# Optimization experiments

Measured on AMD Instinct MI355X. Metric: run time of the kernel, lower is better.

## Reference

```python
import jax, jax.numpy as jnp
import numpy as np

EMBED_DIM = 256
NUM_HEADS = 8
NUM_QUERIES = 448
TEMPERATURE = 10000.0
SCALE = 100.0
EPS = 1e-5
B, N = 1, 512
NUM_CLASSES = 91


def box_rel_encoding(src_boxes, tgt_boxes, eps=EPS):
    # boxes: [B, N, 4] as (cx, cy, w, h)
    xy1, wh1 = src_boxes[..., :2], src_boxes[..., 2:]
    xy2, wh2 = tgt_boxes[..., :2], tgt_boxes[..., 2:]
    delta_xy = jnp.abs(xy1[..., :, None, :] - xy2[..., None, :, :])          # [B,N,N,2]
    delta_xy = jnp.log(delta_xy / (wh1[..., :, None, :] + eps) + 1.0)
    delta_wh = jnp.log((wh1[..., :, None, :] + eps) / (wh2[..., None, :, :] + eps))
    return jnp.concatenate([delta_xy, delta_wh], axis=-1)                    # [B,N,N,4]


def get_sine_pos_embed(pos, num_pos_feats, temperature=TEMPERATURE, scale=SCALE):
    # pos: [..., C]; returns [..., C * num_pos_feats]; exchange_xy=False
    dim_t = jnp.arange(num_pos_feats, dtype=pos.dtype)
    dim_t = temperature ** (2.0 * jnp.floor(dim_t / 2.0) / num_pos_feats)
    x = pos[..., None] * scale / dim_t                                        # [...,C,F]
    emb = jnp.stack([jnp.sin(x[..., 0::2]), jnp.cos(x[..., 1::2])], axis=-1)  # [...,C,F/2,2]
    emb = emb.reshape(x.shape)                                                # [...,C,F]
    return emb.reshape(pos.shape[:-1] + (pos.shape[-1] * num_pos_feats,))


def setup_inputs() -> dict:
    key = jax.random.key(0)
    ks = jax.random.split(key, 9)
    s = 0.02
    return {
        "src_boxes": jax.random.uniform(ks[0], (B, N, 4), jnp.float32, 0.05, 0.95),
        "pred_logits": jax.random.normal(ks[1], (B, N, NUM_CLASSES), jnp.float32),
        "rank_emb": jax.random.normal(ks[2], (NUM_QUERIES, EMBED_DIM), jnp.float32) * s,
        "pre_W": jax.random.normal(ks[3], (EMBED_DIM, EMBED_DIM), jnp.float32) * s,
        "pre_b": jax.random.normal(ks[4], (EMBED_DIM,), jnp.float32) * s,
        "post_W": jax.random.normal(ks[5], (EMBED_DIM, 2 * EMBED_DIM), jnp.float32) * s,
        "post_b": jax.random.normal(ks[6], (EMBED_DIM,), jnp.float32) * s,
        "attn_W": jax.random.normal(ks[7], (NUM_HEADS, EMBED_DIM), jnp.float32) * s,
        "attn_b": jax.random.normal(ks[8], (NUM_HEADS,), jnp.float32) * s,
        "layer_idx": 2,
    }


def reference(src_boxes, pred_logits, rank_emb, pre_W, pre_b, post_W, post_b, attn_W, attn_b, layer_idx):
    num_denoising = N - NUM_QUERIES
    # --- no-grad block: pairwise box relation + rank-ordered gather reorder ---
    base = box_rel_encoding(src_boxes, src_boxes)                            # [B,N,N,4]
    scores = jnp.max(jax.nn.sigmoid(pred_logits[:, num_denoising:]), axis=-1)  # [B,Q]
    order = jnp.argsort(-scores, axis=1)                                      # descending  [B,Q]
    rank_indices = jnp.broadcast_to(jnp.arange(N, dtype=order.dtype), (B, N))
    rank_indices = rank_indices.at[:, num_denoising:].set(order + num_denoising)
    nr = base[:, num_denoising:, num_denoising:]                              # [B,Q,Q,4]
    nr = jnp.take_along_axis(nr, order[:, :, None, None], axis=1)
    nr = jnp.take_along_axis(nr, order[:, None, :, None], axis=2)
    base = base.at[:, num_denoising:, num_denoising:].set(nr)
    base = jax.lax.stop_gradient(base)
    # --- sine positional embedding of relation: [B,N,N,EMBED_DIM] ---
    pos = get_sine_pos_embed(base, EMBED_DIM // 4)
    # --- rank-aware relation: embedding -> pre linear -> pairwise sum ---
    normal_rank = rank_emb @ pre_W.T + pre_b                                  # [Q,E]
    rank_rel = jnp.zeros((B, N, EMBED_DIM), src_boxes.dtype)
    rank_rel = rank_rel.at[:, num_denoising:].set(normal_rank[None])
    rank_rel = rank_rel[:, :, None, :] + rank_rel[:, None, :, :]              # [B,N,N,E]
    relation = jnp.concatenate([pos, rank_rel], axis=-1)                      # [B,N,N,2E]
    relation = relation @ post_W.T + post_b                                   # [B,N,N,E]
    attn = jax.nn.relu(relation @ attn_W.T + attn_b)                          # [B,N,N,H]
    attn = jnp.transpose(attn, (0, 3, 1, 2))                                  # [B,H,N,N]
    return attn, rank_indices
```

## Files before the change

### kernel.cpp

```cpp
#include <hip/hip_runtime.h>
#include <hip/hip_bf16.h>
#include <math.h>

#define NN 512
#define NQ 448
#define ND 64
#define NC 91
#define ED 256
#define NH 8

typedef __attribute__((ext_vector_type(8))) short bf16x8;
typedef __attribute__((ext_vector_type(4))) float f32x4;

struct FreqArg { float fr[32]; };

__device__ int   g_perm[NN];
__device__ float g_c0[NH];
__device__ float g_afull[NN * NH];
__device__ __align__(16) unsigned short g_WB[8 * 64 * 8];

__device__ inline unsigned short f2bfbits(float x) {
    __hip_bfloat16 h = __float2bfloat16(x);
    union { __hip_bfloat16 b; unsigned short u; } cv; cv.b = h; return cv.u;
}

__global__ __launch_bounds__(512) void precomp(const float* __restrict__ logits,
                                               const float* __restrict__ attn_W,
                                               const float* __restrict__ attn_b,
                                               const float* __restrict__ post_W,
                                               const float* __restrict__ post_b,
                                               const float* __restrict__ pre_W,
                                               const float* __restrict__ pre_b,
                                               const float* __restrict__ rank_emb,
                                               float* __restrict__ out2) {
    __shared__ float sAW[ED];
    __shared__ float sFold[512];
    __shared__ float sU2[512];
    __shared__ float sU[ED];
    __shared__ float sc[NQ];
    __shared__ float sB2a;
    int bid = blockIdx.x, t = threadIdx.x;

    if (bid < NH) {
        int h = bid;
        if (t < ED) sAW[t] = attn_W[h * ED + t];
        __syncthreads();

        float m = 0.f;
        const float* pw = post_W + t;
#pragma unroll 16
        for (int c = 0; c < ED; ++c) m = fmaf(sAW[c], pw[(size_t)c * 512], m);
        sFold[t] = m;
        __syncthreads();

        {
            int e = t & 255, half = t >> 8;
            float acc = 0.f;
            const float* pwc = pre_W + (size_t)(half * 128) * ED + e;
#pragma unroll 16
            for (int dl = 0; dl < 128; ++dl)
                acc = fmaf(sFold[256 + half * 128 + dl], pwc[(size_t)dl * ED], acc);
            sU2[half * 256 + e] = acc;
        }
        if (t < 64) {
            float v = 0.f;
#pragma unroll
            for (int k = 0; k < 4; ++k) v = fmaf(sAW[t + 64 * k], post_b[t + 64 * k], v);
            for (int off = 32; off > 0; off >>= 1) v += __shfl_down(v, off, 64);
            if (t == 0) g_c0[h] = attn_b[h] + v;
        } else if (t < 128) {
            int l = t - 64;
            float v = 0.f;
#pragma unroll
            for (int k = 0; k < 4; ++k) v = fmaf(sFold[256 + l + 64 * k], pre_b[l + 64 * k], v);
            for (int off = 32; off > 0; off >>= 1) v += __shfl_down(v, off, 64);
            if (l == 0) sB2a = v;
        }
        if (t < 256) {
            int s = t >> 5, g = (t >> 3) & 3, ii = t & 7;
            int d = g * 64 + ((s * 4 + (ii >> 1)) << 1) + (ii & 1);
            g_WB[s * 512 + (g * 16 + h) * 8 + ii] = f2bfbits(sFold[d]);
        }
        if (t < ND) g_afull[t * NH + h] = 0.f;
        __syncthreads();
        if (t < ED) sU[t] = sU2[t] + sU2[256 + t];
        __syncthreads();

        float b2a = sB2a;
        for (int pass = 0; pass < 14; ++pass) {
            int q = pass * 32 + (t >> 4);
            int sub = t & 15;
            const float* re = rank_emb + (size_t)q * ED;
            float a = 0.f;
#pragma unroll
            for (int kk = 0; kk < 16; ++kk) a = fmaf(re[sub + 16 * kk], sU[sub + 16 * kk], a);
            a += __shfl_xor(a, 1, 64);
            a += __shfl_xor(a, 2, 64);
            a += __shfl_xor(a, 4, 64);
            a += __shfl_xor(a, 8, 64);
            if (sub == 0) g_afull[(size_t)(ND + q) * NH + h] = b2a + a;
        }
    } else {
        for (int v = t; v < 4096; v += 512) {
            int lane = (v >> 3) & 63;
            if ((lane & 15) >= NH) g_WB[v] = 0;
        }
        int W = t >> 6, lane = t & 63;
        for (int qi = 0; qi < 56; ++qi) {
            int q = W * 56 + qi;
            const float* row = logits + (size_t)(ND + q) * NC;
            float m = (lane < NC) ? row[lane] : -INFINITY;
            int c2 = lane + 64;
            if (c2 < NC) m = fmaxf(m, row[c2]);
            for (int off = 32; off > 0; off >>= 1) m = fmaxf(m, __shfl_down(m, off, 64));
            if (lane == 0) sc[q] = m;
        }
        __syncthreads();
        if (t < NQ) {
            float s1 = sc[t];
            int r1 = 0;
            for (int j = 0; j < NQ; ++j) {
                float sj = sc[j];
                r1 += ((sj > s1) || (sj == s1 && j < t)) ? 1 : 0;
            }
            g_perm[ND + r1] = ND + t;
            out2[ND + r1] = (float)(ND + t);
        }
        if (t < ND) {
            g_perm[t] = t;
            out2[t] = (float)t;
        }
    }
}

__global__ __launch_bounds__(256) void relation_main(const float* __restrict__ boxes,
                                                     FreqArg fa,
                                                     float* __restrict__ out) {
    __shared__ bf16x8 sWB[8][64];
    int t = threadIdx.x;
    ((uint4*)sWB)[t]       = ((const uint4*)g_WB)[t];
    ((uint4*)sWB)[t + 256] = ((const uint4*)g_WB)[t + 256];
    __syncthreads();

    int wave = t >> 6, lane = t & 63;
    int g = lane >> 4, r = lane & 15;
    int i = blockIdx.x >> 3;
    int j = ((blockIdx.x & 7) << 6) + (wave << 4) + r;

    int pi = i, pj = j;
    if (i >= ND && j >= ND) { pi = g_perm[i]; pj = g_perm[j]; }
    float4 b1 = ((const float4*)boxes)[pi];
    float4 b2 = ((const float4*)boxes)[pj];
    const float eps = 1e-5f;
    float ft;
    if (g == 0)      ft = logf(fabsf(b1.x - b2.x) / (b1.z + eps) + 1.0f);
    else if (g == 1) ft = logf(fabsf(b1.y - b2.y) / (b1.w + eps) + 1.0f);
    else if (g == 2) ft = logf((b1.z + eps) / (b2.z + eps));
    else             ft = logf((b1.w + eps) / (b2.w + eps));

    f32x4 acc = {0.f, 0.f, 0.f, 0.f};
#pragma unroll
    for (int s = 0; s < 8; ++s) {
        bf16x8 bfrag;
#pragma unroll
        for (int a = 0; a < 4; ++a) {
            float rev = ft * fa.fr[s * 4 + a];
            rev -= floorf(rev);
            float sv = __builtin_amdgcn_sinf(rev);
            float cv = __builtin_amdgcn_cosf(rev);
            bfrag[2 * a]     = (short)f2bfbits(sv);
            bfrag[2 * a + 1] = (short)f2bfbits(cv);
        }
        acc = __builtin_amdgcn_mfma_f32_16x16x32_bf16(sWB[s][lane], bfrag, acc, 0, 0, 0);
    }

    if (g < 2) {
        float4 cb = *(const float4*)(g_c0 + g * 4);
        float4 ai = *(const float4*)(g_afull + i * NH + g * 4);
        float4 aj = *(const float4*)(g_afull + j * NH + g * 4);
        const float* cbp = (const float*)&cb;
        const float* aip = (const float*)&ai;
        const float* ajp = (const float*)&aj;
#pragma unroll
        for (int q = 0; q < 4; ++q) {
            int h = g * 4 + q;
            float v = acc[q] + cbp[q] + aip[q] + ajp[q];
            v = v > 0.f ? v : 0.f;
            out[(size_t)h * (NN * NN) + i * NN + j] = v;
        }
    }
}

extern "C" void kernel_launch(void* const* d_in, const int* in_sizes, int n_in,
                              void* d_out, int out_size, void* d_ws, size_t ws_size,
                              hipStream_t stream) {
    const float* boxes    = (const float*)d_in[0];
    const float* logits   = (const float*)d_in[1];
    const float* rank_emb = (const float*)d_in[2];
    const float* pre_W    = (const float*)d_in[3];
    const float* pre_b    = (const float*)d_in[4];
    const float* post_W   = (const float*)d_in[5];
    const float* post_b   = (const float*)d_in[6];
    const float* attn_W   = (const float*)d_in[7];
    const float* attn_b   = (const float*)d_in[8];
    float* out = (float*)d_out;

    precomp<<<NH + 1, 512, 0, stream>>>(logits, attn_W, attn_b, post_W, post_b,
                                        pre_W, pre_b, rank_emb,
                                        out + (size_t)NH * NN * NN);

    FreqArg fa;
    for (int k = 0; k < 32; ++k)
        fa.fr[k] = (float)(100.0 / (2.0 * M_PI) / pow(10000.0, (double)k / 32.0));

    relation_main<<<4096, 256, 0, stream>>>(boxes, fa, out);
}
```

Baseline: 51.03 us.

## Split precompute across more blocks and move rank projection into tiled main kernel

Measured after the change: 59.90 us. +17.4%, slower.

```diff
diff --git a/kernel.cpp b/kernel.cpp
--- a/kernel.cpp
+++ b/kernel.cpp
@@ -16,7 +16,8 @@
 
 __device__ int   g_perm[NN];
 __device__ float g_c0[NH];
-__device__ float g_afull[NN * NH];
+__device__ float g_u[NH * ED];
+__device__ float g_b2a[NH];
 __device__ __align__(16) unsigned short g_WB[8 * 64 * 8];
 
 __device__ inline unsigned short f2bfbits(float x) {
@@ -24,87 +25,65 @@
     union { __hip_bfloat16 b; unsigned short u; } cv; cv.b = h; return cv.u;
 }
 
-__global__ __launch_bounds__(512) void precomp(const float* __restrict__ logits,
-                                               const float* __restrict__ attn_W,
-                                               const float* __restrict__ attn_b,
-                                               const float* __restrict__ post_W,
-                                               const float* __restrict__ post_b,
-                                               const float* __restrict__ pre_W,
-                                               const float* __restrict__ pre_b,
-                                               const float* __restrict__ rank_emb,
-                                               float* __restrict__ out2) {
+__global__ __launch_bounds__(512) void k1(const float* __restrict__ logits,
+                                          const float* __restrict__ attn_W,
+                                          const float* __restrict__ attn_b,
+                                          const float* __restrict__ post_W,
+                                          const float* __restrict__ post_b,
+                                          const float* __restrict__ pre_W,
+                                          const float* __restrict__ pre_b,
+                                          float* __restrict__ out2) {
     __shared__ float sAW[ED];
-    __shared__ float sFold[512];
-    __shared__ float sU2[512];
-    __shared__ float sU[ED];
+    __shared__ float sHalf[2][ED];
+    __shared__ float sW[ED];
+    __shared__ float sU2[2 * ED];
     __shared__ float sc[NQ];
-    __shared__ float sB2a;
     int bid = blockIdx.x, t = threadIdx.x;
 
-    if (bid < NH) {
-        int h = bid;
+    if (bid < 16) {
+        int h = bid >> 1, part = bid & 1;
         if (t < ED) sAW[t] = attn_W[h * ED + t];
         __syncthreads();
-
+        int dl = t & 255, cp = t >> 8;
         float m = 0.f;
-        const float* pw = post_W + t;
+        const float* pw = post_W + (size_t)(cp * 128) * 512 + part * 256 + dl;
 #pragma unroll 16
-        for (int c = 0; c < ED; ++c) m = fmaf(sAW[c], pw[(size_t)c * 512], m);
-        sFold[t] = m;
+        for (int ci = 0; ci < 128; ++ci) m = fmaf(sAW[cp * 128 + ci], pw[(size_t)ci * 512], m);
+        sHalf[cp][dl] = m;
         __syncthreads();
 
-        {
+        if (part == 0) {
+            if (t < 256) {
+                int s = t >> 5, g = (t >> 3) & 3, ii = t & 7;
+                int d = g * 64 + ((s * 4 + (ii >> 1)) << 1) + (ii & 1);
+                g_WB[s * 512 + (g * 16 + h) * 8 + ii] = f2bfbits(sHalf[0][d] + sHalf[1][d]);
+            }
+            if (h == 0) {
+                for (int v = t; v < 4096; v += 512) {
+                    int lane = (v >> 3) & 63;
+                    if ((lane & 15) >= NH) g_WB[v] = 0;
+                }
+            }
+        } else {
+            if (t < ED) sW[t] = sHalf[0][t] + sHalf[1][t];
+            __syncthreads();
             int e = t & 255, half = t >> 8;
             float acc = 0.f;
             const float* pwc = pre_W + (size_t)(half * 128) * ED + e;
 #pragma unroll 16
-            for (int dl = 0; dl < 128; ++dl)
-                acc = fmaf(sFold[256 + half * 128 + dl], pwc[(size_t)dl * ED], acc);
+            for (int d2 = 0; d2 < 128; ++d2) acc = fmaf(sW[half * 128 + d2], pwc[(size_t)d2 * ED], acc);
             sU2[half * 256 + e] = acc;
-        }
-        if (t < 64) {
-            float v = 0.f;
-#pragma unroll
-            for (int k = 0; k < 4; ++k) v = fmaf(sAW[t + 64 * k], post_b[t + 64 * k], v);
-            for (int off = 32; off > 0; off >>= 1) v += __shfl_down(v, off, 64);
-            if (t == 0) g_c0[h] = attn_b[h] + v;
-        } else if (t < 128) {
-            int l = t - 64;
-            float v = 0.f;
-#pragma unroll
-            for (int k = 0; k < 4; ++k) v = fmaf(sFold[256 + l + 64 * k], pre_b[l + 64 * k], v);
-            for (int off = 32; off > 0; off >>= 1) v += __shfl_down(v, off, 64);
-            if (l == 0) sB2a = v;
-        }
-        if (t < 256) {
-            int s = t >> 5, g = (t >> 3) & 3, ii = t & 7;
-            int d = g * 64 + ((s * 4 + (ii >> 1)) << 1) + (ii & 1);
-            g_WB[s * 512 + (g * 16 + h) * 8 + ii] = f2bfbits(sFold[d]);
-        }
-        if (t < ND) g_afull[t * NH + h] = 0.f;
-        __syncthreads();
-        if (t < ED) sU[t] = sU2[t] + sU2[256 + t];
-        __syncthreads();
-
-        float b2a = sB2a;
-        for (int pass = 0; pass < 14; ++pass) {
-            int q = pass * 32 + (t >> 4);
-            int sub = t & 15;
-            const float* re = rank_emb + (size_t)q * ED;
-            float a = 0.f;
-#pragma unroll
-            for (int kk = 0; kk < 16; ++kk) a = fmaf(re[sub + 16 * kk], sU[sub + 16 * kk], a);
-            a += __shfl_xor(a, 1, 64);
-            a += __shfl_xor(a, 2, 64);
-            a += __shfl_xor(a, 4, 64);
-            a += __shfl_xor(a, 8, 64);
-            if (sub == 0) g_afull[(size_t)(ND + q) * NH + h] = b2a + a;
-        }
-    } else {
-        for (int v = t; v < 4096; v += 512) {
-            int lane = (v >> 3) & 63;
-            if ((lane & 15) >= NH) g_WB[v] = 0;
-        }
+            __syncthreads();
+            if (t < ED) g_u[h * ED + t] = sU2[t] + sU2[256 + t];
+            if (t < 64) {
+                float v = 0.f;
+#pragma unroll
+                for (int k = 0; k < 4; ++k) v = fmaf(sW[t + 64 * k], pre_b[t + 64 * k], v);
+                for (int off = 32; off > 0; off >>= 1) v += __shfl_down(v, off, 64);
+                if (t == 0) g_b2a[h] = v;
+            }
+        }
+    } else if (bid == 16) {
         int W = t >> 6, lane = t & 63;
         for (int qi = 0; qi < 56; ++qi) {
             int q = W * 56 + qi;
@@ -130,63 +109,100 @@
             g_perm[t] = t;
             out2[t] = (float)t;
         }
+    } else {
+        int h = t >> 6, lane = t & 63;
+        float v = 0.f;
+#pragma unroll
+        for (int k = 0; k < 4; ++k) {
+            int c = lane + 64 * k;
+            v = fmaf(attn_W[h * ED + c], post_b[c], v);
+        }
+        for (int off = 32; off > 0; off >>= 1) v += __shfl_down(v, off, 64);
+        if (lane == 0) g_c0[h] = attn_b[h] + v;
     }
 }
 
-__global__ __launch_bounds__(256) void relation_main(const float* __restrict__ boxes,
-                                                     FreqArg fa,
-                                                     float* __restrict__ out) {
+__global__ __launch_bounds__(256) void mainv2(const float* __restrict__ boxes,
+                                              const float* __restrict__ rank_emb,
+                                              FreqArg fa,
+                                              float* __restrict__ out) {
     __shared__ bf16x8 sWB[8][64];
-    int t = threadIdx.x;
+    __shared__ float sU[NH][260];
+    __shared__ float sAf[32][9];
+    __shared__ int   sPerm[32];
+    __shared__ float sB2a[NH], sC0[NH];
+    int t = threadIdx.x, bid = blockIdx.x;
+    int i0 = (bid >> 5) * 16, j0 = (bid & 31) * 16;
+
     ((uint4*)sWB)[t]       = ((const uint4*)g_WB)[t];
     ((uint4*)sWB)[t + 256] = ((const uint4*)g_WB)[t + 256];
+    for (int v = t; v < NH * ED; v += 256) sU[v >> 8][v & 255] = g_u[v];
+    if (t < NH) { sB2a[t] = g_b2a[t]; sC0[t] = g_c0[t]; }
+    if (t < 16) sPerm[t] = g_perm[i0 + t];
+    else if (t < 32) sPerm[t] = g_perm[j0 + (t - 16)];
     __syncthreads();
 
-    int wave = t >> 6, lane = t & 63;
+    {
+        int rr = t >> 3, h = t & 7;
+        int pos = (rr < 16) ? (i0 + rr) : (j0 + (rr - 16));
+        float a = 0.f;
+        if (pos >= ND) {
+            const float* re = rank_emb + (size_t)(pos - ND) * ED;
+            for (int e = 0; e < ED; ++e) a = fmaf(re[e], sU[h][e], a);
+            a += sB2a[h];
+        }
+        sAf[rr][h] = a;
+    }
+    __syncthreads();
+
+    int wv = t >> 6, lane = t & 63;
     int g = lane >> 4, r = lane & 15;
-    int i = blockIdx.x >> 3;
-    int j = ((blockIdx.x & 7) << 6) + (wave << 4) + r;
-
-    int pi = i, pj = j;
-    if (i >= ND && j >= ND) { pi = g_perm[i]; pj = g_perm[j]; }
-    float4 b1 = ((const float4*)boxes)[pi];
-    float4 b2 = ((const float4*)boxes)[pj];
+    bool jdn = (j0 < ND);
+    int j = j0 + r;
+    float4 b2p = ((const float4*)boxes)[j];
+    float4 b2s = jdn ? b2p : ((const float4*)boxes)[sPerm[16 + r]];
+    float4 cb4 = *(const float4*)(sC0 + (g & 1) * 4);
     const float eps = 1e-5f;
-    float ft;
-    if (g == 0)      ft = logf(fabsf(b1.x - b2.x) / (b1.z + eps) + 1.0f);
-    else if (g == 1) ft = logf(fabsf(b1.y - b2.y) / (b1.w + eps) + 1.0f);
-    else if (g == 2) ft = logf((b1.z + eps) / (b2.z + eps));
-    else             ft = logf((b1.w + eps) / (b2.w + eps));
-
-    f32x4 acc = {0.f, 0.f, 0.f, 0.f};
-#pragma unroll
-    for (int s = 0; s < 8; ++s) {
-        bf16x8 bfrag;
-#pragma unroll
-        for (int a = 0; a < 4; ++a) {
-            float rev = ft * fa.fr[s * 4 + a];
-            rev -= floorf(rev);
-            float sv = __builtin_amdgcn_sinf(rev);
-            float cv = __builtin_amdgcn_cosf(rev);
-            bfrag[2 * a]     = (short)f2bfbits(sv);
-            bfrag[2 * a + 1] = (short)f2bfbits(cv);
-        }
-        acc = __builtin_amdgcn_mfma_f32_16x16x32_bf16(sWB[s][lane], bfrag, acc, 0, 0, 0);
-    }
-
-    if (g < 2) {
-        float4 cb = *(const float4*)(g_c0 + g * 4);
-        float4 ai = *(const float4*)(g_afull + i * NH + g * 4);
-        float4 aj = *(const float4*)(g_afull + j * NH + g * 4);
-        const float* cbp = (const float*)&cb;
-        const float* aip = (const float*)&ai;
-        const float* ajp = (const float*)&aj;
-#pragma unroll
-        for (int q = 0; q < 4; ++q) {
-            int h = g * 4 + q;
-            float v = acc[q] + cbp[q] + aip[q] + ajp[q];
-            v = v > 0.f ? v : 0.f;
-            out[(size_t)h * (NN * NN) + i * NN + j] = v;
+
+#pragma unroll
+    for (int gi = 0; gi < 4; ++gi) {
+        int iloc = wv * 4 + gi;
+        int i = i0 + iloc;
+        bool prm = (i >= ND) && !jdn;
+        float4 b1 = ((const float4*)boxes)[prm ? sPerm[iloc] : i];
+        float4 b2 = prm ? b2s : b2p;
+
+        float ft;
+        if (g == 0)      ft = logf(fabsf(b1.x - b2.x) / (b1.z + eps) + 1.0f);
+        else if (g == 1) ft = logf(fabsf(b1.y - b2.y) / (b1.w + eps) + 1.0f);
+        else if (g == 2) ft = logf((b1.z + eps) / (b2.z + eps));
+        else             ft = logf((b1.w + eps) / (b2.w + eps));
+
+        f32x4 acc = {0.f, 0.f, 0.f, 0.f};
+#pragma unroll
+        for (int s = 0; s < 8; ++s) {
+            bf16x8 bfrag;
+#pragma unroll
+            for (int a = 0; a < 4; ++a) {
+                float rev = ft * fa.fr[s * 4 + a];
+                rev -= floorf(rev);
+                float sv = __builtin_amdgcn_sinf(rev);
+                float cv = __builtin_amdgcn_cosf(rev);
+                bfrag[2 * a]     = (short)f2bfbits(sv);
+                bfrag[2 * a + 1] = (short)f2bfbits(cv);
+            }
+            acc = __builtin_amdgcn_mfma_f32_16x16x32_bf16(sWB[s][lane], bfrag, acc, 0, 0, 0);
+        }
+
+        if (g < 2) {
+            const float* cbp = (const float*)&cb4;
+#pragma unroll
+            for (int qq = 0; qq < 4; ++qq) {
+                int h = g * 4 + qq;
+                float v = acc[qq] + cbp[qq] + sAf[iloc][h] + sAf[16 + r][h];
+                v = v > 0.f ? v : 0.f;
+                out[(size_t)h * (NN * NN) + (size_t)i * NN + j] = v;
+            }
         }
     }
 }
@@ -205,13 +221,12 @@
     const float* attn_b   = (const float*)d_in[8];
     float* out = (float*)d_out;
 
-    precomp<<<NH + 1, 512, 0, stream>>>(logits, attn_W, attn_b, post_W, post_b,
-                                        pre_W, pre_b, rank_emb,
-                                        out + (size_t)NH * NN * NN);
+    k1<<<18, 512, 0, stream>>>(logits, attn_W, attn_b, post_W, post_b,
+                               pre_W, pre_b, out + (size_t)NH * NN * NN);
 
     FreqArg fa;
     for (int k = 0; k < 32; ++k)
         fa.fr[k] = (float)(100.0 / (2.0 * M_PI) / pow(10000.0, (double)k / 32.0));
 
-    relation_main<<<4096, 256, 0, stream>>>(boxes, fa, out);
-}
+    mainv2<<<1024, 256, 0, stream>>>(boxes, rank_emb, fa, out);
+}
```
